# Optimization experiments

Measured on AMD Instinct MI355X. Metric: run time of the kernel, lower is better.

Reference implementation:

```python
import jax, jax.numpy as jnp
import numpy as np

REG = 5
SCORE_THRESH = 0.05
NMS_THRESH = 0.5
DET_PER_IMG = 100
BBOX_XFORM_CLIP = float(np.log(1000.0 / 16.0))
WEIGHTS = (10.0, 10.0, 5.0, 5.0, 10.0)  # (wx, wy, ww, wh, wa)
MAXV = 8  # max vertices of intersection of two convex quads


def decode(rel_codes, boxes):
    # rel_codes: [N, C*5], boxes: [N, 5] = (xc, yc, w, h, angle_deg)
    xc, yc, w, h, a = (boxes[:, i] for i in range(5))
    wx, wy, ww, wh, wa = WEIGHTS
    dx = rel_codes[:, 0::REG] / wx
    dy = rel_codes[:, 1::REG] / wy
    dw = jnp.minimum(rel_codes[:, 2::REG] / ww, BBOX_XFORM_CLIP)
    dh = jnp.minimum(rel_codes[:, 3::REG] / wh, BBOX_XFORM_CLIP)
    da = rel_codes[:, 4::REG] / wa
    px = dx * w[:, None] + xc[:, None]
    py = dy * h[:, None] + yc[:, None]
    pw = jnp.exp(dw) * w[:, None]
    ph = jnp.exp(dh) * h[:, None]
    pa = da * (180.0 / np.pi) + a[:, None]
    return jnp.stack([px, py, pw, ph, pa], axis=2).reshape(rel_codes.shape[0], -1)


def box_corners(b):
    # b: [..., 5] -> CCW corners [..., 4, 2]
    xc, yc, w, h, a = jnp.moveaxis(b, -1, 0)
    t = a * (np.pi / 180.0)
    c, s = jnp.cos(t), jnp.sin(t)
    lx = jnp.stack([-w, w, w, -w], -1) * 0.5
    ly = jnp.stack([-h, -h, h, h], -1) * 0.5
    x = xc[..., None] + lx * c[..., None] - ly * s[..., None]
    y = yc[..., None] + lx * s[..., None] + ly * c[..., None]
    return jnp.stack([x, y], -1)


def _clip_one(polyA, polyB):
    # Sutherland-Hodgman: clip quad A by CCW quad B; return intersection area.
    poly = jnp.zeros((MAXV, 2), polyA.dtype).at[:4].set(polyA)
    n0 = jnp.int32(4)
    idx = jnp.arange(MAXV)

    def clip_edge(carry, edge):
        poly, n = carry
        p1, p2 = edge[0], edge[1]
        valid = idx < n
        nxt = poly[jnp.where(idx + 1 < n, idx + 1, 0)]
        cur = poly
        e = p2 - p1
        sc = e[0] * (cur[:, 1] - p1[1]) - e[1] * (cur[:, 0] - p1[0])
        sn = e[0] * (nxt[:, 1] - p1[1]) - e[1] * (nxt[:, 0] - p1[0])
        in_c, in_n = sc >= 0, sn >= 0
        denom = sc - sn
        t = sc / jnp.where(jnp.abs(denom) > 1e-8, denom, 1.0)
        inter = cur + t[:, None] * (nxt - cur)
        emit_c = valid & in_c
        emit_i = valid & (in_c ^ in_n)
        pts = jnp.stack([cur, inter], 1).reshape(2 * MAXV, 2)
        flags = jnp.stack([emit_c, emit_i], 1).reshape(2 * MAXV)
        pos = jnp.where(flags, jnp.cumsum(flags) - 1, 2 * MAXV)
        newpoly = jnp.zeros((2 * MAXV + 1, 2), poly.dtype).at[pos].set(pts)[:MAXV]
        newn = jnp.minimum(jnp.sum(flags), MAXV).astype(jnp.int32)
        return (newpoly, newn), None

    edges = jnp.stack([polyB, jnp.roll(polyB, -1, axis=0)], 1)  # [4, 2, 2]
    (poly, n), _ = jax.lax.scan(clip_edge, (poly, n0), edges)
    valid = idx < n
    nxt = poly[jnp.where(idx + 1 < n, idx + 1, 0)]
    cross = poly[:, 0] * nxt[:, 1] - nxt[:, 0] * poly[:, 1]
    area = 0.5 * jnp.abs(jnp.sum(jnp.where(valid, cross, 0.0)))
    return jnp.where(n >= 3, area, 0.0)


def rotated_iou_matrix(boxes):
    # boxes: [N, 5] -> IoU [N, N]
    corners = box_corners(boxes)
    areas = boxes[:, 2] * boxes[:, 3]
    inter = jax.vmap(lambda ca: jax.vmap(lambda cb: _clip_one(ca, cb))(corners))(corners)
    union = areas[:, None] + areas[None, :] - inter
    return inter / jnp.maximum(union, 1e-8)


def greedy_nms(iou, valid):
    N = iou.shape[-1]
    ar = jnp.arange(N)

    def body(i, keep):
        sup = keep[i] & (iou[i] > NMS_THRESH) & (ar > i)
        return keep & ~sup

    keep = jax.lax.fori_loop(0, N, body, valid)
    return keep & (jnp.cumsum(keep) <= DET_PER_IMG)  # post_nms_top_n


def process_image(scores, proposals_dec):
    # scores: [N, C], proposals_dec: [N, C*5]; skip background class 0
    N, C = scores.shape
    fg = C - 1
    s = scores[:, 1:].T                                       # [fg, N]
    b = proposals_dec.reshape(N, C, REG)[:, 1:].transpose(1, 0, 2)  # [fg, N, 5]
    valid = s > SCORE_THRESH
    s_m = jnp.where(valid, s, -jnp.inf)
    order = jnp.argsort(-s_m, axis=1)                         # per-class descending sort
    s_sorted = jnp.take_along_axis(s_m, order, 1)
    b_sorted = jnp.take_along_axis(b, jnp.broadcast_to(order[:, :, None], b.shape), 1)
    v_sorted = jnp.take_along_axis(valid, order, 1)
    iou = jax.lax.stop_gradient(jax.vmap(rotated_iou_matrix)(b_sorted))  # [fg, N, N]
    keep = jax.vmap(greedy_nms)(iou, v_sorted)
    s_kept = jnp.where(keep, s_sorted, -jnp.inf)
    # cross-class top-k (limit to detections_per_img)
    top_s, top_idx = jax.lax.top_k(s_kept.reshape(-1), DET_PER_IMG)
    top_b = b_sorted.reshape(-1, REG)[top_idx]
    ok = jnp.isfinite(top_s)
    out = jnp.concatenate([top_b, top_s[:, None]], 1)         # (xc,yc,w,h,angle,score)
    return jnp.where(ok[:, None], out, 0.0)                   # [DET_PER_IMG, 6]


def setup_inputs() -> dict:
    key = jax.random.key(0)
    k1, k2, k3 = jax.random.split(key, 3)
    B, N, C = 2, 512, 16
    class_logits = jax.random.normal(k1, (B, N, C), jnp.float32)
    box_regression = jax.random.normal(k2, (B, N, C * REG), jnp.float32)
    u = jax.random.uniform(k3, (B, N, 5), jnp.float32)
    proposal_boxes = jnp.stack([
        u[..., 0] * 1024.0,          # xc
        u[..., 1] * 1024.0,          # yc
        16.0 + u[..., 2] * 240.0,    # w
        16.0 + u[..., 3] * 240.0,    # h
        u[..., 4] * 180.0 - 90.0,    # angle (deg)
    ], -1)
    return {"class_logits": class_logits, "box_regression": box_regression,
            "proposal_boxes": proposal_boxes}


def reference(class_logits, box_regression, proposal_boxes):
    B = class_logits.shape[0]
    probs = jax.nn.softmax(class_logits, -1)                  # [B, N, C]
    dec = jax.vmap(decode)(box_regression, proposal_boxes)    # [B, N, C*5]
    return jnp.stack([process_image(probs[i], dec[i]) for i in range(B)])  # [B, 100, 6]
```

## Files before the change

### kernel.cpp

```cpp
#include <hip/hip_runtime.h>

#define FG 15
#define NPROP 512
#define NCLS 16
#define NCI 30
#define SCORE_T 0.05f
#define NMS_T 0.5f
#define DETS 100
#define STRIPES 8
#define NWAVES 8
#define WCAP 512

typedef unsigned long long u64;
typedef unsigned int u32;

__device__ __forceinline__ unsigned sortable_f32(float f) {
  unsigned u = __float_as_uint(f);
  return u ^ ((u >> 31) ? 0xFFFFFFFFu : 0x80000000u);
}

#define CLIP_EMIT(V, VALIDEXPR, CX, CY, NX, NY)                                \
  {                                                                            \
    bool valid = (VALIDEXPR);                                                  \
    float cx = (CX), cy = (CY), nx = (NX), ny = (NY);                          \
    float sc = ex * (cy - p1y) - ey * (cx - p1x);                              \
    float sn = ex * (ny - p1y) - ey * (nx - p1x);                              \
    bool ic = sc >= 0.f, inn = sn >= 0.f;                                      \
    float den = sc - sn;                                                       \
    float dsel = (fabsf(den) > 1e-8f) ? den : 1.f;                             \
    float tt = sc * __builtin_amdgcn_rcpf(dsel);                               \
    float qx = cx + tt * (nx - cx);                                            \
    float qy = cy + tt * (ny - cy);                                            \
    bool fC = valid && ic;                                                     \
    bool fI = valid && (ic != inn);                                            \
    _Pragma("unroll") for (int o = 0; o < 8; ++o) if (o <= 2 * (V)) {          \
      bool wr = fC && (m == o);                                                \
      ox[o] = wr ? cx : ox[o];                                                 \
      oy[o] = wr ? cy : oy[o];                                                 \
    }                                                                          \
    m += fC ? 1 : 0;                                                           \
    _Pragma("unroll") for (int o = 0; o < 8; ++o) if (o <= 2 * (V) + 1) {      \
      bool wr = fI && (m == o);                                                \
      ox[o] = wr ? qx : ox[o];                                                 \
      oy[o] = wr ? qy : oy[o];                                                 \
    }                                                                          \
    m += fI ? 1 : 0;                                                           \
  }

__device__ __forceinline__ float inter_area_fast(const float (&Ax)[4], const float (&Ay)[4],
                                                 const float (&Bx)[4], const float (&By)[4]) {
  float inx[8], iny[8];
  int n = 4;
#pragma unroll
  for (int v = 0; v < 4; ++v) {
    inx[v] = Ax[v]; iny[v] = Ay[v];
    inx[v + 4] = 0.f; iny[v + 4] = 0.f;
  }
#pragma unroll
  for (int e = 0; e < 4; ++e) {
    int e2 = (e + 1) & 3;
    float p1x = Bx[e], p1y = By[e];
    float ex = Bx[e2] - p1x, ey = By[e2] - p1y;
    float ox[8], oy[8];
    int m = 0;
#pragma unroll
    for (int o = 0; o < 8; ++o) { ox[o] = 0.f; oy[o] = 0.f; }
    if (e == 0) {
#pragma unroll
      for (int v = 0; v < 4; ++v) {
        CLIP_EMIT(v, true, inx[v], iny[v], inx[(v + 1) & 3], iny[(v + 1) & 3]);
      }
    } else {
#pragma unroll
      for (int v = 0; v < 8; ++v) {
        bool wrap = (v + 1 >= n);
        CLIP_EMIT(v, v < n, inx[v], iny[v],
                  wrap ? inx[0] : inx[(v + 1) & 7],
                  wrap ? iny[0] : iny[(v + 1) & 7]);
      }
    }
    n = (m < 8) ? m : 8;
#pragma unroll
    for (int o = 0; o < 8; ++o) { inx[o] = ox[o]; iny[o] = oy[o]; }
  }
  float s = 0.f;
#pragma unroll
  for (int v = 0; v < 8; ++v) {
    bool valid = v < n;
    bool wrap = (v + 1 >= n);
    float axx = inx[v], ayy = iny[v];
    float bxx = wrap ? inx[0] : inx[(v + 1) & 7];
    float byy = wrap ? iny[0] : iny[(v + 1) & 7];
    float cr = axx * byy - bxx * ayy;
    s += valid ? cr : 0.f;
  }
  float area = 0.5f * fabsf(s);
  return (n >= 3) ? area : 0.f;
}

__global__ void __launch_bounds__(512) k_pipe(
    const float* __restrict__ logits, const float* __restrict__ regr,
    const float* __restrict__ prop,
    float* __restrict__ ssort, float* __restrict__ bsort,
    u64* __restrict__ mask) {
  int ci = blockIdx.x;
  int s = blockIdx.y;
  int b = ci / FG, c = ci - b * FG + 1;
  int tid = threadIdx.x, lane = tid & 63, wv = tid >> 6;

  __shared__ __align__(16) u64 key2[NPROP + 8];
  __shared__ int rmap[NPROP];
  __shared__ int cnt[NWAVES];
  __shared__ __align__(16) float crn[NPROP][8];
  __shared__ float4 aabb[NPROP];
  __shared__ float areaL[NPROP];
  __shared__ u32 stage[NWAVES][WCAP];
  __shared__ int wcnts[NWAVES];
  __shared__ u64 lmask2[NPROP];

  lmask2[tid] = 0ull;

  float sc, bb[5];
  u64 k;
  {
#pragma clang fp contract(off)
    int g = b * NPROP + tid;
    const float4* lg4 = (const float4*)(logits + g * NCLS);
    float l[NCLS];
#pragma unroll
    for (int q4 = 0; q4 < 4; ++q4) {
      float4 v = lg4[q4];
      l[q4 * 4 + 0] = v.x; l[q4 * 4 + 1] = v.y;
      l[q4 * 4 + 2] = v.z; l[q4 * 4 + 3] = v.w;
    }
    float mx = -INFINITY;
#pragma unroll
    for (int q = 0; q < NCLS; ++q) mx = fmaxf(mx, l[q]);
    float sum = 0.f, ec = 0.f;
#pragma unroll
    for (int q = 0; q < NCLS; ++q) {
      float e = expf(l[q] - mx);
      sum += e;
      if (q == c) ec = e;
    }
    sc = ec / sum;
    const float* pb = prop + g * 5;
    float xc = pb[0], yc = pb[1], w = pb[2], h = pb[3], a = pb[4];
    const float* r = regr + g * 80 + c * 5;
    float dx = r[0] / 10.0f;
    float dy = r[1] / 10.0f;
    float dw = fminf(r[2] / 5.0f, 4.135166556742356f);
    float dh = fminf(r[3] / 5.0f, 4.135166556742356f);
    float da = r[4] / 10.0f;
    bb[0] = dx * w + xc;
    bb[1] = dy * h + yc;
    bb[2] = expf(dw) * w;
    bb[3] = expf(dh) * h;
    bb[4] = da * 57.29577951308232f + a;
    float m = (sc > SCORE_T) ? sc : -INFINITY;
    k = ((u64)(~sortable_f32(m)) << 32) | (u32)tid;
  }
  bool val = sc > SCORE_T;
  u64 bal = __ballot(val);
  if (lane == 0) cnt[wv] = (int)__popcll(bal);
  __syncthreads();
  int base = 0, V = 0;
#pragma unroll
  for (int w = 0; w < NWAVES; ++w) {
    int cw = cnt[w];
    base += (w < wv) ? cw : 0;
    V += cw;
  }
  if (val) key2[base + (int)__popcll(bal & ((1ull << lane) - 1ull))] = k;
  int Vpad = (V + 7) & ~7;
  if (tid < Vpad - V) key2[V + tid] = ~0ull;
  __syncthreads();

  if (tid < V) {
    u64 myk = key2[tid];
    int rank = 0;
    const ulonglong2* k2 = (const ulonglong2*)key2;
#pragma unroll 4
    for (int m = 0; m < Vpad / 2; ++m) {
      ulonglong2 kk = k2[m];
      rank += (kk.x < myk) ? 1 : 0;
      rank += (kk.y < myk) ? 1 : 0;
    }
    rmap[(int)(myk & 0xFFFFFFFFull)] = rank;
    if (s == 0) {
      u32 so = ~(u32)(myk >> 32);
      ssort[ci * NPROP + rank] = __uint_as_float(so ^ 0x80000000u);
    }
  }
  if (tid >= V && s == 0) ssort[ci * NPROP + tid] = -INFINITY;
  __syncthreads();

  if (val) {
    int r = rmap[tid];
    {
      float t = bb[4] * 0.017453292519943295f;
      float cs = __cosf(t), sn = __sinf(t);
      float hw = bb[2] * 0.5f, hh = bb[3] * 0.5f;
      float lx[4] = {-hw, hw, hw, -hw};
      float ly[4] = {-hh, -hh, hh, hh};
      float X[4], Y[4];
#pragma unroll
      for (int q = 0; q < 4; ++q) {
        X[q] = bb[0] + lx[q] * cs - ly[q] * sn;
        Y[q] = bb[1] + lx[q] * sn + ly[q] * cs;
      }
#pragma unroll
      for (int q = 0; q < 4; ++q) { crn[r][q] = X[q]; crn[r][4 + q] = Y[q]; }
      float xmn = fminf(fminf(X[0], X[1]), fminf(X[2], X[3]));
      float xmx = fmaxf(fmaxf(X[0], X[1]), fmaxf(X[2], X[3]));
      float ymn = fminf(fminf(Y[0], Y[1]), fminf(Y[2], Y[3]));
      float ymx = fmaxf(fmaxf(Y[0], Y[1]), fmaxf(Y[2], Y[3]));
      aabb[r] = make_float4(xmn, ymn, xmx, ymx);
      areaL[r] = bb[2] * bb[3];
      if (s == 0) {
        float* dst = bsort + ((size_t)ci * NPROP + r) * 5;
#pragma unroll
        for (int q = 0; q < 5; ++q) dst[q] = bb[q];
      }
    }
  }
  __syncthreads();

  {
    int nch = (V + 63) >> 6;
    int wcnt = 0;
    for (int t = wv;; t += NWAVES) {
      int i = s + STRIPES * t;
      if (i >= V) break;
      float4 ai = aabb[i];
      float Ai = areaL[i];
      for (int ch = i >> 6; ch < nch; ++ch) {
        int j = (ch << 6) | lane;
        bool pass = false;
        if (j > i && j < V) {
          float4 aj = aabb[j];
          float ix = fminf(ai.z, aj.z) - fmaxf(ai.x, aj.x);
          float iy = fminf(ai.w, aj.w) - fmaxf(ai.y, aj.y);
          float ov = fmaxf(ix, 0.f) * fmaxf(iy, 0.f);
          pass = ov > 0.33f * (Ai + areaL[j]);
        }
        u64 bal2 = __ballot(pass);
        if (pass) {
          int pos = wcnt + (int)__popcll(bal2 & ((1ull << lane) - 1ull));
          if (pos < WCAP) stage[wv][pos] = ((u32)i << 9) | (u32)j;
        }
        wcnt += (int)__popcll(bal2);
      }
    }
    if (lane == 0) wcnts[wv] = wcnt < WCAP ? wcnt : WCAP;
  }
  __syncthreads();

  {
    int c0 = wcnts[0], c1 = wcnts[1], c2 = wcnts[2], c3 = wcnts[3];
    int c4 = wcnts[4], c5 = wcnts[5], c6 = wcnts[6], c7 = wcnts[7];
    int p1 = c0, p2 = p1 + c1, p3 = p2 + c2, p4 = p3 + c3;
    int p5 = p4 + c4, p6 = p5 + c5, p7 = p6 + c6;
    int total = p7 + c7;
    for (int p = tid; p < total; p += 512) {
      int r = (p >= p1) + (p >= p2) + (p >= p3) + (p >= p4) +
              (p >= p5) + (p >= p6) + (p >= p7);
      u32 w = 0;
      switch (r) {
        case 0: w = stage[0][p]; break;
        case 1: w = stage[1][p - p1]; break;
        case 2: w = stage[2][p - p2]; break;
        case 3: w = stage[3][p - p3]; break;
        case 4: w = stage[4][p - p4]; break;
        case 5: w = stage[5][p - p5]; break;
        case 6: w = stage[6][p - p6]; break;
        default: w = stage[7][p - p7]; break;
      }
      int i = w >> 9, j = w & 511;
      float4 a0 = *(const float4*)&crn[i][0];
      float4 a1 = *(const float4*)&crn[i][4];
      float4 b0 = *(const float4*)&crn[j][0];
      float4 b1 = *(const float4*)&crn[j][4];
      float Ax[4] = {a0.x, a0.y, a0.z, a0.w};
      float Ay[4] = {a1.x, a1.y, a1.z, a1.w};
      float Bx[4] = {b0.x, b0.y, b0.z, b0.w};
      float By[4] = {b1.x, b1.y, b1.z, b1.w};
      float inter = inter_area_fast(Ax, Ay, Bx, By);
      float areaA = areaL[i];
      float areaB = areaL[j];
      float uni = (areaA + areaB) - inter;
      float iou = inter / fmaxf(uni, 1e-8f);
      if (iou > NMS_T)
        atomicOr(&lmask2[(((i - s) >> 3) << 3) | (j >> 6)], 1ull << (j & 63));
    }
  }
  __syncthreads();

  mask[((size_t)ci * NPROP + s + STRIPES * (tid >> 3)) * 8 + (tid & 7)] = lmask2[tid];
}

__global__ void __launch_bounds__(256) k_nms(
    const float* __restrict__ ssort, const u64* __restrict__ mask,
    u64* __restrict__ kkey) {
  int ci = blockIdx.x;
  int b = ci / FG, cfg = ci - b * FG;
  __shared__ u64 lmask[(NPROP + 4) * 8];
  __shared__ u64 keptw[8];
  __shared__ int vcnt8[8];
  __shared__ int wpre[8];
  int tid = threadIdx.x, lane = tid & 63, wv = tid >> 6;
  const float* ss = ssort + ci * NPROP;
  for (int chunk = wv; chunk < 8; chunk += 4) {
    u64 bal = __ballot(ss[(chunk << 6) | lane] > SCORE_T);
    if (lane == 0) vcnt8[chunk] = (int)__popcll(bal);
  }
  __syncthreads();
  int V = 0;
#pragma unroll
  for (int w = 0; w < 8; ++w) V += vcnt8[w];
  for (int x = tid; x < V * 8; x += 256)
    lmask[x] = mask[(size_t)ci * NPROP * 8 + x];
  if (tid < 32) lmask[V * 8 + tid] = 0ull;
  __syncthreads();
  if (tid == 0) {
    u64 rem[8] = {0, 0, 0, 0, 0, 0, 0, 0};
    u64 kept[8] = {0, 0, 0, 0, 0, 0, 0, 0};
    u64 buf[4][8];
#pragma unroll
    for (int d = 0; d < 4; ++d)
#pragma unroll
      for (int w = 0; w < 8; ++w) buf[d][w] = lmask[d * 8 + w];
    int kc = 0;
    bool stop = (V == 0);
#pragma unroll
    for (int w8 = 0; w8 < 8; ++w8) {
      int lim = V - (w8 << 6);
      lim = lim > 64 ? 64 : lim;
      if (!stop && lim > 0) {
        int lim4 = (lim + 3) & ~3;
        for (int bp4 = 0; bp4 < lim4 && !stop; bp4 += 4) {
#pragma unroll
          for (int d = 0; d < 4; ++d) {
            int bp = bp4 + d;
            int i = (w8 << 6) | bp;
            if (bp < lim && !stop) {
              if (!((rem[w8] >> bp) & 1ull)) {
                kept[w8] |= 1ull << bp;
#pragma unroll
                for (int w = 0; w < 8; ++w) rem[w] |= buf[d][w];
                if (++kc >= DETS) stop = true;
              }
            }
#pragma unroll
            for (int w = 0; w < 8; ++w) buf[d][w] = lmask[(i + 4) * 8 + w];
          }
        }
      }
    }
#pragma unroll
    for (int w = 0; w < 8; ++w) keptw[w] = kept[w];
    int acc = 0;
#pragma unroll
    for (int w = 0; w < 8; ++w) { wpre[w] = acc; acc += (int)__popcll(keptw[w]); }
  }
  __syncthreads();
  for (int i = tid; i < NPROP; i += 256) {
    u64 kw = keptw[i >> 6];
    if ((kw >> (i & 63)) & 1ull) {
      int rank = wpre[i >> 6] + (int)__popcll(kw & ((1ull << (i & 63)) - 1ull));
      float s = ss[i];
      u32 hi = __float_as_uint(s) ^ 0x80000000u;
      u32 flat = (u32)(cfg * NPROP + i);
      kkey[ci * 128 + rank] = ((u64)hi << 32) | (u32)(~flat);
    }
  }
  int total = wpre[7] + (int)__popcll(keptw[7]);
  for (int r = tid; r < 128; r += 256)
    if (r >= total) kkey[ci * 128 + r] = 0ull;
}

__global__ void __launch_bounds__(1024) k_topk(
    const u64* __restrict__ kkey,
    const float* __restrict__ bsort,
    float* __restrict__ out) {
  int b = blockIdx.x;
  __shared__ u64 lk[FG * 128];
  __shared__ u64 res[DETS];
  for (int x = threadIdx.x; x < FG * 128; x += 1024) lk[x] = kkey[b * FG * 128 + x];
  for (int x = threadIdx.x; x < DETS; x += 1024) res[x] = 0ull;
  __syncthreads();
  for (int x = threadIdx.x; x < FG * 128; x += 1024) {
    u64 key = lk[x];
    if (key == 0ull) continue;
    int rank = 0;
#pragma unroll
    for (int c = 0; c < FG; ++c) {
      const u64* a = &lk[c * 128];
      int pos = 0;
#pragma unroll
      for (int st = 64; st > 0; st >>= 1)
        pos += (a[pos + st - 1] > key) ? st : 0;
      rank += pos + ((a[pos] > key) ? 1 : 0);
    }
    if (rank < DETS) res[rank] = key;
  }
  __syncthreads();
  if (threadIdx.x < DETS) {
    u64 key = res[threadIdx.x];
    float* o = out + ((size_t)b * DETS + threadIdx.x) * 6;
    if (key == 0ull) {
#pragma unroll
      for (int q = 0; q < 6; ++q) o[q] = 0.f;
    } else {
      u32 flat = ~(u32)(key & 0xFFFFFFFFull);
      int cfg = flat >> 9, pos = flat & 511;
      const float* bx = bsort + (((size_t)b * FG + cfg) * NPROP + pos) * 5;
#pragma unroll
      for (int q = 0; q < 5; ++q) o[q] = bx[q];
      o[5] = __uint_as_float((u32)(key >> 32) ^ 0x80000000u);
    }
  }
}

extern "C" void kernel_launch(void* const* d_in, const int* in_sizes, int n_in,
                              void* d_out, int out_size, void* d_ws, size_t ws_size,
                              hipStream_t stream) {
  const float* logits = (const float*)d_in[0];
  const float* regr   = (const float*)d_in[1];
  const float* prop   = (const float*)d_in[2];
  float* out = (float*)d_out;

  float* ssort = (float*)d_ws;
  float* bsort = ssort + NCI * NPROP;
  u64* kkey    = (u64*)(bsort + NCI * NPROP * 5);
  u64* mask    = kkey + NCI * 128;

  hipLaunchKernelGGL(k_pipe, dim3(NCI, STRIPES), dim3(512), 0, stream,
                     logits, regr, prop, ssort, bsort, mask);
  hipLaunchKernelGGL(k_nms, dim3(NCI), dim3(256), 0, stream, ssort, mask, kkey);
  hipLaunchKernelGGL(k_topk, dim3(2), dim3(1024), 0, stream, kkey, bsort, out);
}
```

Measured before the change: 45.29 us.

## Fuse top-k selection into NMS kernel via last-block atomic counter

Merges the per-image top-k kernel into the NMS kernel. Each block bumps a per-image atomic counter after writing its kept keys, and the last of the image's 15 blocks does the cross-class rank selection and writes the output. This removes one kernel launch and its inter-kernel gap. In exchange it adds a memset launch for the counters, and the top-k step now runs with 256 threads instead of 1024, so it serialises more.

```diff
diff --git a/kernel.cpp b/kernel.cpp
--- a/kernel.cpp
+++ b/kernel.cpp
@@ -299,17 +299,21 @@
   mask[((size_t)ci * NPROP + s + STRIPES * (tid >> 3)) * 8 + (tid & 7)] = lmask2[tid];
 }
 
-__global__ void __launch_bounds__(256) k_nms(
+__global__ void __launch_bounds__(256) k_nmstk(
     const float* __restrict__ ssort, const u64* __restrict__ mask,
-    u64* __restrict__ kkey) {
+    const float* __restrict__ bsort,
+    u64* __restrict__ kkey, int* __restrict__ done,
+    float* __restrict__ out) {
   int ci = blockIdx.x;
   int b = ci / FG, cfg = ci - b * FG;
-  __shared__ u64 lmask[(NPROP + 4) * 8];
+  __shared__ __align__(16) char arena[(NPROP + 4) * 8 * 8];
   __shared__ u64 keptw[8];
   __shared__ int vcnt8[8];
   __shared__ int wpre[8];
+  __shared__ int lastsh;
   int tid = threadIdx.x, lane = tid & 63, wv = tid >> 6;
   const float* ss = ssort + ci * NPROP;
+  u64* lmask = (u64*)arena;
   for (int chunk = wv; chunk < 8; chunk += 4) {
     u64 bal = __ballot(ss[(chunk << 6) | lane] > SCORE_T);
     if (lane == 0) vcnt8[chunk] = (int)__popcll(bal);
@@ -377,25 +381,27 @@
   int total = wpre[7] + (int)__popcll(keptw[7]);
   for (int r = tid; r < 128; r += 256)
     if (r >= total) kkey[ci * 128 + r] = 0ull;
-}
-
-__global__ void __launch_bounds__(1024) k_topk(
-    const u64* __restrict__ kkey,
-    const float* __restrict__ bsort,
-    float* __restrict__ out) {
-  int b = blockIdx.x;
-  __shared__ u64 lk[FG * 128];
-  __shared__ u64 res[DETS];
-  for (int x = threadIdx.x; x < FG * 128; x += 1024) lk[x] = kkey[b * FG * 128 + x];
-  for (int x = threadIdx.x; x < DETS; x += 1024) res[x] = 0ull;
-  __syncthreads();
-  for (int x = threadIdx.x; x < FG * 128; x += 1024) {
+  __syncthreads();
+
+  __threadfence();
+  if (tid == 0) lastsh = atomicAdd(&done[b], 1);
+  __syncthreads();
+  if (lastsh != FG - 1) return;
+
+  __threadfence();
+  u64* lk = (u64*)arena;
+  u64* res = (u64*)(arena + FG * 128 * 8);
+  __syncthreads();
+  for (int x = tid; x < FG * 128; x += 256) lk[x] = kkey[b * FG * 128 + x];
+  for (int x = tid; x < DETS; x += 256) res[x] = 0ull;
+  __syncthreads();
+  for (int x = tid; x < FG * 128; x += 256) {
     u64 key = lk[x];
     if (key == 0ull) continue;
     int rank = 0;
 #pragma unroll
-    for (int c = 0; c < FG; ++c) {
-      const u64* a = &lk[c * 128];
+    for (int cc = 0; cc < FG; ++cc) {
+      const u64* a = &lk[cc * 128];
       int pos = 0;
 #pragma unroll
       for (int st = 64; st > 0; st >>= 1)
@@ -405,16 +411,16 @@
     if (rank < DETS) res[rank] = key;
   }
   __syncthreads();
-  if (threadIdx.x < DETS) {
-    u64 key = res[threadIdx.x];
-    float* o = out + ((size_t)b * DETS + threadIdx.x) * 6;
+  if (tid < DETS) {
+    u64 key = res[tid];
+    float* o = out + ((size_t)b * DETS + tid) * 6;
     if (key == 0ull) {
 #pragma unroll
       for (int q = 0; q < 6; ++q) o[q] = 0.f;
     } else {
       u32 flat = ~(u32)(key & 0xFFFFFFFFull);
-      int cfg = flat >> 9, pos = flat & 511;
-      const float* bx = bsort + (((size_t)b * FG + cfg) * NPROP + pos) * 5;
+      int cfg2 = flat >> 9, pos = flat & 511;
+      const float* bx = bsort + (((size_t)b * FG + cfg2) * NPROP + pos) * 5;
 #pragma unroll
       for (int q = 0; q < 5; ++q) o[q] = bx[q];
       o[5] = __uint_as_float((u32)(key >> 32) ^ 0x80000000u);
@@ -434,9 +440,11 @@
   float* bsort = ssort + NCI * NPROP;
   u64* kkey    = (u64*)(bsort + NCI * NPROP * 5);
   u64* mask    = kkey + NCI * 128;
-
+  int* done    = (int*)(mask + (size_t)NCI * NPROP * 8);
+
+  hipMemsetAsync(done, 0, 2 * sizeof(int), stream);
   hipLaunchKernelGGL(k_pipe, dim3(NCI, STRIPES), dim3(512), 0, stream,
                      logits, regr, prop, ssort, bsort, mask);
-  hipLaunchKernelGGL(k_nms, dim3(NCI), dim3(256), 0, stream, ssort, mask, kkey);
-  hipLaunchKernelGGL(k_topk, dim3(2), dim3(1024), 0, stream, kkey, bsort, out);
+  hipLaunchKernelGGL(k_nmstk, dim3(NCI), dim3(256), 0, stream,
+                     ssort, mask, bsort, kkey, done, out);
 }
```

Result: slower. 59.88 us (+32.2%).
